# Optimization experiments

Measured on AMD Instinct MI355X. Metric: run time of the kernel, lower is better.

Reference implementation:

```python
import jax, jax.numpy as jnp
import numpy as np

B, T, F, H, E = 256, 512, 32, 512, 32
NUM_TICKERS, PREDICT_DAYS = 5000, 30


def setup_inputs() -> dict:
    key = jax.random.key(0)
    ks = jax.random.split(key, 16)
    s = 0.05  # small init scale for stability
    return {
        "ticker_id": jax.random.randint(ks[0], (B,), 0, NUM_TICKERS),
        "sequence": jax.random.normal(ks[1], (B, T, F), jnp.float32),
        "embed_table": jax.random.normal(ks[2], (NUM_TICKERS, E), jnp.float32) * s,
        "Wih0": jax.random.normal(ks[3], (3 * H, F), jnp.float32) * s,
        "Whh0": jax.random.normal(ks[4], (3 * H, H), jnp.float32) * s,
        "bih0": jax.random.normal(ks[5], (3 * H,), jnp.float32) * s,
        "bhh0": jax.random.normal(ks[6], (3 * H,), jnp.float32) * s,
        "Wih1": jax.random.normal(ks[7], (3 * H, H), jnp.float32) * s,
        "Whh1": jax.random.normal(ks[8], (3 * H, H), jnp.float32) * s,
        "bih1": jax.random.normal(ks[9], (3 * H,), jnp.float32) * s,
        "bhh1": jax.random.normal(ks[10], (3 * H,), jnp.float32) * s,
        "fc1_w": jax.random.normal(ks[11], (H, H + E), jnp.float32) * s,
        "fc1_b": jax.random.normal(ks[12], (H,), jnp.float32) * s,
        "fc2_w": jax.random.normal(ks[13], (PREDICT_DAYS, H), jnp.float32) * s,
        "fc2_b": jax.random.normal(ks[14], (PREDICT_DAYS,), jnp.float32) * s,
    }


def _gru_layer(x, Wih, Whh, bih, bhh):
    """Standard torch-convention GRU layer. x: (B,T,in) -> (B,T,H), h_last (B,H).
    Gate packing along 3H axis: [r, z, n]."""
    Hs = Whh.shape[1]
    # precompute input projections for all timesteps in one GEMM
    gx = jnp.einsum('btf,gf->tbg', x, Wih) + bih  # (T,B,3H)

    def step(h, gxt):
        gh = h @ Whh.T + bhh                         # (B,3H)
        r = jax.nn.sigmoid(gxt[:, :Hs] + gh[:, :Hs])
        z = jax.nn.sigmoid(gxt[:, Hs:2 * Hs] + gh[:, Hs:2 * Hs])
        n = jnp.tanh(gxt[:, 2 * Hs:] + r * gh[:, 2 * Hs:])
        h_new = (1.0 - z) * n + z * h
        return h_new, h_new

    h0 = jnp.zeros((x.shape[0], Hs), x.dtype)
    h_last, ys = jax.lax.scan(step, h0, gx)          # ys: (T,B,H)
    return jnp.moveaxis(ys, 0, 1), h_last


def reference(ticker_id, sequence, embed_table, Wih0, Whh0, bih0, bhh0,
              Wih1, Whh1, bih1, bhh1, fc1_w, fc1_b, fc2_w, fc2_b):
    out0, _ = _gru_layer(sequence, Wih0, Whh0, bih0, bhh0)
    _, h_last = _gru_layer(out0, Wih1, Whh1, bih1, bhh1)   # top-layer final hidden (B,H)
    embed = embed_table[ticker_id]                          # (B,E)
    h = jnp.concatenate([h_last, embed], axis=1)            # (B,H+E)
    h = jax.nn.relu(h @ fc1_w.T + fc1_b)                    # dropout is eval no-op
    return h @ fc2_w.T + fc2_b                              # (B, predict_days)
```

## Files before the change

### kernel.cpp

```cpp
#include <hip/hip_runtime.h>
#include <hip/hip_bf16.h>


namespace {
constexpr int kB  = 256;
constexpr int kT  = 512;
constexpr int kF  = 32;
constexpr int kH  = 512;
constexpr int kE  = 32;
constexpr int kPD = 30;

constexpr int GBLK = 256;
constexpr int NTHR = 256;
constexpr int RG   = 32;
constexpr int HB   = 16;

constexpr int IMG  = kB * kH * 2;
constexpr int RING = 8;

constexpr int PART_OFF = 0;
constexpr int PARTN    = 1536;
constexpr int LDSB     = 98304;
static_assert(LDSB <= 160 * 1024, "LDS overflow");

constexpr size_t WS_CNT   = 0;
constexpr size_t WS_TOTAL = 1024;
constexpr size_t WS_FB    = 1152;
constexpr size_t WS_FLG1  = 2048;
constexpr size_t WS_FLG0  = 4096;
constexpr size_t WS_H0B   = 65536;
constexpr size_t WS_H1B   = WS_H0B + (size_t)RING * IMG;
constexpr size_t WS_H1F   = WS_H1B + (size_t)RING * IMG;
constexpr size_t WS_INIT  = WS_H1F;

typedef __bf16 bf16_t;
typedef __bf16 bf16x8 __attribute__((ext_vector_type(8)));
typedef float  f32x4  __attribute__((ext_vector_type(4)));

#define MFMA __builtin_amdgcn_mfma_f32_16x16x32_bf16
#define LDSF4(p) (*(__attribute__((address_space(3))) f32x4*)(p))

#define WAITVM(N)                                              \
  do {                                                         \
    asm volatile("s_waitcnt vmcnt(" #N ")" ::: "memory");      \
    __builtin_amdgcn_sched_barrier(0);                         \
  } while (0)

__device__ __forceinline__ float sigmoid_f(float x) {
  return 1.f / (1.f + __expf(-x));
}
__device__ __forceinline__ float tanh_f(float x) {
  float a = fabsf(x);
  float e = __expf(-2.f * a);
  float t = (1.f - e) / (1.f + e);
  return copysignf(t, x);
}

__device__ __forceinline__ bf16x8 ld16a(const char* p) {
  bf16x8 v;
  asm volatile("global_load_dwordx4 %0, %1, off"
               : "=v"(v) : "v"(p) : "memory");
  return v;
}

__device__ __forceinline__ bf16x8 fragf(const float* p) {
  bf16x8 t;
#pragma unroll
  for (int j = 0; j < 8; ++j) t[j] = (bf16_t)p[j];
  return t;
}

__device__ __forceinline__ bf16x8 ld16_mall(const bf16_t* p) {
  const unsigned long long* q = (const unsigned long long*)p;
  unsigned long long lo =
      __hip_atomic_load(q, __ATOMIC_RELAXED, __HIP_MEMORY_SCOPE_AGENT);
  unsigned long long hi =
      __hip_atomic_load(q + 1, __ATOMIC_RELAXED, __HIP_MEMORY_SCOPE_AGENT);
  union { unsigned long long u[2]; bf16x8 v; } x;
  x.u[0] = lo; x.u[1] = hi;
  return x.v;
}

__device__ __forceinline__ void st2_mall(bf16_t* p, float v) {
  bf16_t b = (bf16_t)v;
  unsigned short bits = __builtin_bit_cast(unsigned short, b);
  __hip_atomic_store((unsigned short*)p, bits, __ATOMIC_RELAXED,
                     __HIP_MEMORY_SCOPE_AGENT);
}
template <bool XL>
__device__ __forceinline__ void st2x(bf16_t* p, float v) {
  if constexpr (XL) *p = (bf16_t)v;
  else st2_mall(p, v);
}

__device__ __forceinline__ void drain_stores() {
  asm volatile("s_waitcnt vmcnt(0)" ::: "memory");
}

__device__ __forceinline__ unsigned ld_flag_sc1(const unsigned* p) {
  unsigned v;
  asm volatile("global_load_dword %0, %1, off sc1\n\ts_waitcnt vmcnt(0)"
               : "=v"(v) : "v"(p) : "memory");
  return v;
}

template <bool XL>
__device__ __forceinline__ void poll_flags(const unsigned* base, int idx,
                                           unsigned tgt) {
  const unsigned* fp = base + idx;
  long guard = 0;
  if constexpr (XL) {
    for (;;) {
      unsigned v = ld_flag_sc1(fp);
      if (__all((int)(v >= tgt))) break;
      if (++guard > (1L << 22)) break;
    }
  } else {
    for (;;) {
      unsigned v = __hip_atomic_load(fp, __ATOMIC_RELAXED,
                                     __HIP_MEMORY_SCOPE_AGENT);
      if (__all((int)(v >= tgt))) break;
      __builtin_amdgcn_s_sleep(1);
      if (++guard > (1L << 20)) break;
    }
  }
}

template <bool XL>
__device__ __forceinline__ void flag_post(unsigned* p, unsigned tgt) {
  if constexpr (XL) {
    *(volatile unsigned*)p = tgt;
  } else {
    __hip_atomic_store(p, tgt, __ATOMIC_RELAXED, __HIP_MEMORY_SCOPE_AGENT);
  }
}
}


#define L0_ISSUE(buf, base)                                         \
  _Pragma("unroll") for (int j = 0; j < 4; ++j)                     \
      buf[j] = ld16a(hsrc + (base + j) * 1024)
#define L0_MFMA(buf, base)                                          \
  _Pragma("unroll") for (int j = 0; j < 4; ++j) {                   \
    aR  = MFMA(buf[j], f0[0][base + j], aR, 0, 0, 0);               \
    aZ  = MFMA(buf[j], f0[1][base + j], aZ, 0, 0, 0);               \
    aNH = MFMA(buf[j], f0[2][base + j], aNH, 0, 0, 0);              \
  }
#define L1_ISSUE(b0, b1, base)                                      \
  _Pragma("unroll") for (int j = 0; j < 4; ++j) {                   \
    b0[j] = ld16a(hsrc + (base + j) * 1024);                        \
    b1[j] = ld16a(hsrc + 16384 + (base + j) * 1024);                \
  }
#define L1_MFMA(acc0, acc1, acc2, w, b0, b1, base)                  \
  _Pragma("unroll") for (int j = 0; j < 4; ++j) {                   \
    acc0[0] = MFMA(b0[j], w[0][base + j], acc0[0], 0, 0, 0);        \
    acc0[1] = MFMA(b1[j], w[0][base + j], acc0[1], 0, 0, 0);        \
    acc1[0] = MFMA(b0[j], w[1][base + j], acc1[0], 0, 0, 0);        \
    acc1[1] = MFMA(b1[j], w[1][base + j], acc1[1], 0, 0, 0);        \
    acc2[0] = MFMA(b0[j], w[2][base + j], acc2[0], 0, 0, 0);        \
    acc2[1] = MFMA(b1[j], w[2][base + j], acc2[1], 0, 0, 0);        \
  }

template <bool XL>
__device__ __attribute__((noinline)) void role_l0(
    const float* __restrict__ seq, const float* __restrict__ Whh0,
    const float* __restrict__ Wih0, bf16_t* __restrict__ h0b,
    unsigned* __restrict__ flg0p, int g, int slot, int lane, int rbase,
    int rt, int c, float b0r, float b0z, float b0nx, float b0nh) {
  const int lm = lane & 15, lq = lane >> 4, koff = lq * 8;
  const int arow = rbase + rt * 16 + lm;

  bf16x8 f0[3][17];
#pragma unroll
  for (int gg = 0; gg < 3; ++gg) {
    const float* wh = Whh0 + (size_t)(gg * kH + c) * kH + koff;
#pragma unroll
    for (int kc = 0; kc < 16; ++kc) f0[gg][kc] = fragf(wh + kc * 32);
    f0[gg][16] = fragf(Wih0 + (size_t)(gg * kH + c) * kF + koff);
  }
  float h0m[4] = {0.f, 0.f, 0.f, 0.f};

  const int kcb = slot >> 1;
  const int lq2 = ((slot & 1) << 1) | (lm >> 3);
  const int stoff = ((g * 2 + rt) * 16 + kcb) * 1024 +
                    ((lq2 << 4) + lq * 4) * 16 + (lm & 7) * 2;
  const int tbase = (g * 2 + rt) * 16 * 1024;

  for (int s = 0; s <= kT; ++s) {
    const int pr = (s + RING - 1) & (RING - 1), pw = s & (RING - 1);
    if (s < kT) {
      const float* xp = seq + ((size_t)arow * kT + s) * kF + koff;
      float xs[8];
#pragma unroll
      for (int j = 0; j < 8; ++j) xs[j] = xp[j];
      if (s > 0) poll_flags<XL>(flg0p, lane, (unsigned)s);
      if constexpr (XL) {
        if ((s & (RING - 1)) == 0) asm volatile("buffer_inv" ::: "memory");
      }
      f32x4 aR{0,0,0,0}, aZ{0,0,0,0}, aNH{0,0,0,0}, aNX{0,0,0,0};
      const char* hsrc = (const char*)h0b + pr * IMG + tbase + lane * 16;
      if constexpr (XL) {
        bf16x8 cA[4], cB[4];
        L0_ISSUE(cA, 0);
        L0_ISSUE(cB, 4);
        WAITVM(4);
        L0_MFMA(cA, 0);
        L0_ISSUE(cA, 8);
        WAITVM(4);
        L0_MFMA(cB, 4);
        L0_ISSUE(cB, 12);
        WAITVM(4);
        L0_MFMA(cA, 8);
        WAITVM(0);
        L0_MFMA(cB, 12);
      } else {
#pragma unroll
        for (int kc = 0; kc < 16; ++kc) {
          bf16x8 a = ld16_mall((const bf16_t*)(hsrc + kc * 1024));
          aR  = MFMA(a, f0[0][kc], aR, 0, 0, 0);
          aZ  = MFMA(a, f0[1][kc], aZ, 0, 0, 0);
          aNH = MFMA(a, f0[2][kc], aNH, 0, 0, 0);
        }
      }
      {
        bf16x8 ax;
#pragma unroll
        for (int j = 0; j < 8; ++j) ax[j] = (bf16_t)xs[j];
        aR  = MFMA(ax, f0[0][16], aR, 0, 0, 0);
        aZ  = MFMA(ax, f0[1][16], aZ, 0, 0, 0);
        aNX = MFMA(ax, f0[2][16], aNX, 0, 0, 0);
      }
      char* hnb = (char*)h0b + pw * IMG;
#pragma unroll
      for (int i = 0; i < 4; ++i) {
        float r = sigmoid_f(aR[i] + b0r);
        float z = sigmoid_f(aZ[i] + b0z);
        float n = tanh_f((aNX[i] + b0nx) + r * (aNH[i] + b0nh));
        float hn = (1.f - z) * n + z * h0m[i];
        h0m[i] = hn;
        st2x<XL>((bf16_t*)(hnb + stoff + i * 16), hn);
      }
      drain_stores();
      if (lane == 0) flag_post<XL>(flg0p + rt * 32 + slot, (unsigned)(s + 1));
    }
    __syncthreads();
    if constexpr (!XL) __syncthreads();
  }
}

template <bool XL>
__device__ __attribute__((noinline)) void role_l1h(
    const float* __restrict__ Whh1, bf16_t* __restrict__ h1b,
    float* __restrict__ h1f, unsigned* __restrict__ flg1p, int slot,
    float* part, int g, int lane, int rbase, int c,
    float b1r, float b1z, float b1nx, float b1nh) {
  const int lm = lane & 15, lq = lane >> 4, koff = lq * 8;
  bf16x8 fh[3][16];
#pragma unroll
  for (int gg = 0; gg < 3; ++gg) {
    const float* wh = Whh1 + (size_t)(gg * kH + c) * kH + koff;
#pragma unroll
    for (int kc = 0; kc < 16; ++kc) fh[gg][kc] = fragf(wh + kc * 32);
  }
  float h1m[2][4] = {{0,0,0,0},{0,0,0,0}};

  const int kcb = slot >> 1;
  const int lq2 = ((slot & 1) << 1) | (lm >> 3);
  const int st0 = (g * 2 * 16 + kcb) * 1024 +
                  ((lq2 << 4) + lq * 4) * 16 + (lm & 7) * 2;
  const int tbase = g * 2 * 16 * 1024;

  for (int s = 0; s <= kT; ++s) {
    const int pr = (s + RING - 1) & (RING - 1), pw = s & (RING - 1);
    f32x4 cR[2], cZ[2], cNH[2];
#pragma unroll
    for (int rt = 0; rt < 2; ++rt) {
      cR[rt] = f32x4{0,0,0,0}; cZ[rt] = f32x4{0,0,0,0}; cNH[rt] = f32x4{0,0,0,0};
    }
    if (s >= 1) {
      poll_flags<XL>(flg1p, lane & 31, (unsigned)s);
      if constexpr (XL) {
        if ((s & (RING - 1)) == 0) asm volatile("buffer_inv" ::: "memory");
      }
      const char* hsrc = (const char*)h1b + pr * IMG + tbase + lane * 16;
      if constexpr (XL) {
        bf16x8 a0A[4], a1A[4], a0B[4], a1B[4];
        L1_ISSUE(a0A, a1A, 0);
        L1_ISSUE(a0B, a1B, 4);
        WAITVM(8);
        L1_MFMA(cR, cZ, cNH, fh, a0A, a1A, 0);
        L1_ISSUE(a0A, a1A, 8);
        WAITVM(8);
        L1_MFMA(cR, cZ, cNH, fh, a0B, a1B, 4);
        L1_ISSUE(a0B, a1B, 12);
        WAITVM(8);
        L1_MFMA(cR, cZ, cNH, fh, a0A, a1A, 8);
        WAITVM(0);
        L1_MFMA(cR, cZ, cNH, fh, a0B, a1B, 12);
      } else {
#pragma unroll
        for (int kc = 0; kc < 16; ++kc) {
          bf16x8 a0 = ld16_mall((const bf16_t*)(hsrc + kc * 1024));
          bf16x8 a1 = ld16_mall((const bf16_t*)(hsrc + 16384 + kc * 1024));
          cR[0]  = MFMA(a0, fh[0][kc], cR[0], 0,0,0);
          cR[1]  = MFMA(a1, fh[0][kc], cR[1], 0,0,0);
          cZ[0]  = MFMA(a0, fh[1][kc], cZ[0], 0,0,0);
          cZ[1]  = MFMA(a1, fh[1][kc], cZ[1], 0,0,0);
          cNH[0] = MFMA(a0, fh[2][kc], cNH[0],0,0,0);
          cNH[1] = MFMA(a1, fh[2][kc], cNH[1],0,0,0);
        }
      }
    }
    __syncthreads();
    if (s >= 1) {
      float* pb = part + (s & 1) * PARTN;
      char* hnb = (char*)h1b + pw * IMG;
#pragma unroll
      for (int rt = 0; rt < 2; ++rt) {
        f32x4 pR  = LDSF4(pb + ((rt * 3 + 0) * 64 + lane) * 4);
        f32x4 pZ  = LDSF4(pb + ((rt * 3 + 1) * 64 + lane) * 4);
        f32x4 pNX = LDSF4(pb + ((rt * 3 + 2) * 64 + lane) * 4);
#pragma unroll
        for (int i = 0; i < 4; ++i) {
          float r = sigmoid_f(cR[rt][i] + pR[i] + b1r);
          float z = sigmoid_f(cZ[rt][i] + pZ[i] + b1z);
          float n = tanh_f((pNX[i] + b1nx) + r * (cNH[rt][i] + b1nh));
          float hn = (1.f - z) * n + z * h1m[rt][i];
          h1m[rt][i] = hn;
          if (s < kT) st2x<XL>((bf16_t*)(hnb + st0 + rt * 16384 + i * 16), hn);
          else        h1f[(rbase + rt * 16 + lq * 4 + i) * kH + c] = hn;
        }
      }
    }
    if (s < kT) {
      drain_stores();
      if (lane == 0) flag_post<XL>(flg1p + slot, (unsigned)(s + 1));
    }
    if constexpr (!XL) {
      if (s < kT) poll_flags<XL>(flg1p, lane & 31, (unsigned)(s + 1));
      __syncthreads();
    }
  }
}

template <bool XL>
__device__ __attribute__((noinline)) void role_l1x(
    const float* __restrict__ Wih1, bf16_t* __restrict__ h0b,
    float* part, unsigned* __restrict__ flg0p, int g, int lane, int c) {
  const int lq = lane >> 4, koff = lq * 8;
  bf16x8 fx[3][16];
#pragma unroll
  for (int gg = 0; gg < 3; ++gg) {
    const float* wi = Wih1 + (size_t)(gg * kH + c) * kH + koff;
#pragma unroll
    for (int kc = 0; kc < 16; ++kc) fx[gg][kc] = fragf(wi + kc * 32);
  }
  const int tbase = g * 2 * 16 * 1024;

  for (int s = 0; s <= kT; ++s) {
    const int pr = (s + RING - 1) & (RING - 1);
    if (s >= 1) {
      poll_flags<XL>(flg0p, lane, (unsigned)s);
      if constexpr (XL) {
        if ((s & (RING - 1)) == 0) asm volatile("buffer_inv" ::: "memory");
      }
      f32x4 xR[2], xZ[2], xNX[2];
#pragma unroll
      for (int rt = 0; rt < 2; ++rt) {
        xR[rt] = f32x4{0,0,0,0}; xZ[rt] = f32x4{0,0,0,0}; xNX[rt] = f32x4{0,0,0,0};
      }
      const char* hsrc = (const char*)h0b + pr * IMG + tbase + lane * 16;
      if constexpr (XL) {
        bf16x8 a0A[4], a1A[4], a0B[4], a1B[4];
        L1_ISSUE(a0A, a1A, 0);
        L1_ISSUE(a0B, a1B, 4);
        WAITVM(8);
        L1_MFMA(xR, xZ, xNX, fx, a0A, a1A, 0);
        L1_ISSUE(a0A, a1A, 8);
        WAITVM(8);
        L1_MFMA(xR, xZ, xNX, fx, a0B, a1B, 4);
        L1_ISSUE(a0B, a1B, 12);
        WAITVM(8);
        L1_MFMA(xR, xZ, xNX, fx, a0A, a1A, 8);
        WAITVM(0);
        L1_MFMA(xR, xZ, xNX, fx, a0B, a1B, 12);
      } else {
#pragma unroll
        for (int kc = 0; kc < 16; ++kc) {
          bf16x8 a0 = ld16_mall((const bf16_t*)(hsrc + kc * 1024));
          bf16x8 a1 = ld16_mall((const bf16_t*)(hsrc + 16384 + kc * 1024));
          xR[0]  = MFMA(a0, fx[0][kc], xR[0], 0,0,0);
          xR[1]  = MFMA(a1, fx[0][kc], xR[1], 0,0,0);
          xZ[0]  = MFMA(a0, fx[1][kc], xZ[0], 0,0,0);
          xZ[1]  = MFMA(a1, fx[1][kc], xZ[1], 0,0,0);
          xNX[0] = MFMA(a0, fx[2][kc], xNX[0],0,0,0);
          xNX[1] = MFMA(a1, fx[2][kc], xNX[1],0,0,0);
        }
      }
      float* pb = part + (s & 1) * PARTN;
#pragma unroll
      for (int rt = 0; rt < 2; ++rt) {
        LDSF4(pb + ((rt * 3 + 0) * 64 + lane) * 4) = xR[rt];
        LDSF4(pb + ((rt * 3 + 1) * 64 + lane) * 4) = xZ[rt];
        LDSF4(pb + ((rt * 3 + 2) * 64 + lane) * 4) = xNX[rt];
      }
    }
    __syncthreads();
    if constexpr (!XL) __syncthreads();
  }
}

__launch_bounds__(NTHR, 1)
__global__ void gru_persistent(
    const float* __restrict__ seq,
    const float* __restrict__ Wih0, const float* __restrict__ Whh0,
    const float* __restrict__ bih0, const float* __restrict__ bhh0,
    const float* __restrict__ Wih1, const float* __restrict__ Whh1,
    const float* __restrict__ bih1, const float* __restrict__ bhh1,
    char* __restrict__ ws) {
  extern __shared__ char smem[];
  float* part = (float*)(smem + PART_OFF);
  __shared__ unsigned sh_enc;

  const int tid = threadIdx.x;

  if (tid == 0) {
    unsigned xcd;
    asm("s_getreg_b32 %0, hwreg(HW_REG_XCC_ID)" : "=s"(xcd));
    xcd &= 7;
    unsigned* cnt   = (unsigned*)(ws + WS_CNT) + xcd * 32;
    unsigned* total = (unsigned*)(ws + WS_TOTAL);
    unsigned* fb    = (unsigned*)(ws + WS_FB);
    unsigned slot = __hip_atomic_fetch_add(cnt, 1u, __ATOMIC_RELAXED,
                                           __HIP_MEMORY_SCOPE_AGENT);
    if (slot >= 32)
      __hip_atomic_store(fb, 1u, __ATOMIC_RELAXED, __HIP_MEMORY_SCOPE_AGENT);
    __hip_atomic_fetch_add(total, 1u, __ATOMIC_RELAXED,
                           __HIP_MEMORY_SCOPE_AGENT);
    long guard = 0;
    while (__hip_atomic_load(total, __ATOMIC_RELAXED,
                             __HIP_MEMORY_SCOPE_AGENT) < (unsigned)GBLK) {
      __builtin_amdgcn_s_sleep(1);
      if (++guard > (1L << 24)) break;
    }
    unsigned f = __hip_atomic_load(fb, __ATOMIC_RELAXED,
                                   __HIP_MEMORY_SCOPE_AGENT);
    sh_enc = (f << 31) | (xcd << 8) | (slot & 255);
  }
  __syncthreads();
  const unsigned enc = sh_enc;
  const bool fallback = (enc >> 31) != 0;
  const int g    = fallback ? (blockIdx.x & 7)  : (int)((enc >> 8) & 7);
  const int slot = fallback ? (blockIdx.x >> 3) : (int)(enc & 255);
  const int hs   = slot * HB;

  const int lm = tid & 15;
  const int c = hs + lm;
  const float b0r  = bih0[c] + bhh0[c];
  const float b0z  = bih0[kH + c] + bhh0[kH + c];
  const float b0nx = bih0[2 * kH + c];
  const float b0nh = bhh0[2 * kH + c];
  const float b1r  = bih1[c] + bhh1[c];
  const float b1z  = bih1[kH + c] + bhh1[kH + c];
  const float b1nx = bih1[2 * kH + c];
  const float b1nh = bhh1[2 * kH + c];

  bf16_t* h0b = (bf16_t*)(ws + WS_H0B);
  bf16_t* h1b = (bf16_t*)(ws + WS_H1B);
  float*  h1f = (float*)(ws + WS_H1F);
  unsigned* flg1p = (unsigned*)(ws + WS_FLG1) + g * 32;
  unsigned* flg0p = (unsigned*)(ws + WS_FLG0) + g * 64;
  const int wv   = tid >> 6;
  const int lane = tid & 63;
  const int rbase = g * RG;

  if (!fallback) {
    if (wv == 0)
      role_l0<true>(seq, Whh0, Wih0, h0b, flg0p, g, slot, lane, rbase, 0, c,
                    b0r, b0z, b0nx, b0nh);
    else if (wv == 2)
      role_l0<true>(seq, Whh0, Wih0, h0b, flg0p, g, slot, lane, rbase, 1, c,
                    b0r, b0z, b0nx, b0nh);
    else if (wv == 1)
      role_l1h<true>(Whh1, h1b, h1f, flg1p, slot, part, g, lane, rbase, c,
                     b1r, b1z, b1nx, b1nh);
    else
      role_l1x<true>(Wih1, h0b, part, flg0p, g, lane, c);
  } else {
    if (wv == 0)
      role_l0<false>(seq, Whh0, Wih0, h0b, flg0p, g, slot, lane, rbase, 0, c,
                     b0r, b0z, b0nx, b0nh);
    else if (wv == 2)
      role_l0<false>(seq, Whh0, Wih0, h0b, flg0p, g, slot, lane, rbase, 1, c,
                     b0r, b0z, b0nx, b0nh);
    else if (wv == 1)
      role_l1h<false>(Whh1, h1b, h1f, flg1p, slot, part, g, lane, rbase, c,
                      b1r, b1z, b1nx, b1nh);
    else
      role_l1x<false>(Wih1, h0b, part, flg0p, g, lane, c);
  }
}

__global__ void head_kernel(const float* __restrict__ h1,
                            const int* __restrict__ ticker,
                            const float* __restrict__ etab,
                            const float* __restrict__ fc1w,
                            const float* __restrict__ fc1b,
                            const float* __restrict__ fc2w,
                            const float* __restrict__ fc2b,
                            float* __restrict__ out) {
  __shared__ float xin[4][kH + kE];
  __shared__ float y1[4][kH];
  const int tid = threadIdx.x;
  const int b0 = blockIdx.x * 4;

  for (int idx = tid; idx < 4 * (kH + kE); idx += 256) {
    const int r = idx / (kH + kE), k = idx % (kH + kE);
    const int b = b0 + r;
    xin[r][k] = (k < kH) ? h1[b * kH + k] : etab[ticker[b] * kE + (k - kH)];
  }
  __syncthreads();

#pragma unroll
  for (int jj = 0; jj < 2; ++jj) {
    const int j = tid + jj * 256;
    const float* wr = fc1w + j * (kH + kE);
    float a0 = 0.f, a1 = 0.f, a2 = 0.f, a3 = 0.f;
    for (int k = 0; k < kH + kE; ++k) {
      const float w = wr[k];
      a0 += w * xin[0][k];
      a1 += w * xin[1][k];
      a2 += w * xin[2][k];
      a3 += w * xin[3][k];
    }
    const float bb = fc1b[j];
    y1[0][j] = fmaxf(a0 + bb, 0.f);
    y1[1][j] = fmaxf(a1 + bb, 0.f);
    y1[2][j] = fmaxf(a2 + bb, 0.f);
    y1[3][j] = fmaxf(a3 + bb, 0.f);
  }
  __syncthreads();

  if (tid < 4 * kPD) {
    const int r = tid / kPD, j = tid % kPD;
    const float* wr = fc2w + j * kH;
    float acc = fc2b[j];
    for (int k = 0; k < kH; ++k) acc += wr[k] * y1[r][k];
    out[(b0 + r) * kPD + j] = acc;
  }
}

extern "C" void kernel_launch(void* const* d_in, const int* in_sizes, int n_in,
                              void* d_out, int out_size, void* d_ws,
                              size_t ws_size, hipStream_t stream) {
  (void)in_sizes; (void)n_in; (void)out_size; (void)ws_size;

  const int*   ticker = (const int*)d_in[0];
  const float* seq    = (const float*)d_in[1];
  const float* etab   = (const float*)d_in[2];
  const float* Wih0   = (const float*)d_in[3];
  const float* Whh0   = (const float*)d_in[4];
  const float* bih0   = (const float*)d_in[5];
  const float* bhh0   = (const float*)d_in[6];
  const float* Wih1   = (const float*)d_in[7];
  const float* Whh1   = (const float*)d_in[8];
  const float* bih1   = (const float*)d_in[9];
  const float* bhh1   = (const float*)d_in[10];
  const float* fc1w   = (const float*)d_in[11];
  const float* fc1b   = (const float*)d_in[12];
  const float* fc2w   = (const float*)d_in[13];
  const float* fc2b   = (const float*)d_in[14];

  char* ws = (char*)d_ws;
  (void)hipMemsetAsync(ws, 0, WS_INIT, stream);

  gru_persistent<<<GBLK, NTHR, LDSB, stream>>>(
      seq, Wih0, Whh0, bih0, bhh0, Wih1, Whh1, bih1, bhh1, ws);

  head_kernel<<<kB / 4, 256, 0, stream>>>((const float*)(ws + WS_H1F), ticker,
                                          etab, fc1w, fc1b, fc2w, fc2b,
                                          (float*)d_out);
}
```

Before: 2.178 ms.

## Replace per-step block barriers with LDS flag handoff and ring-reuse global flags

Drops the per-timestep __syncthreads that coupled the layer-0, layer-1 hidden and layer-1 input waves in the fast path. The layer-1 partial-sum exchange now uses LDS ready/consumed counters, and layer 0 waits on a new global flag array before overwriting ring slots, so waves can run ahead up to the ring depth. It also issues buffer_inv every step instead of every eighth. The intent is to remove barrier stalls between roles on the recurrent critical path, at the cost of extra flag polling, more cache invalidations and added risk of memory-ordering bugs.

```diff
diff --git a/kernel.cpp b/kernel.cpp
--- a/kernel.cpp
+++ b/kernel.cpp
@@ -20,6 +20,7 @@
 
 constexpr int PART_OFF = 0;
 constexpr int PARTN    = 1536;
+constexpr int PF_OFF   = 16384;
 constexpr int LDSB     = 98304;
 static_assert(LDSB <= 160 * 1024, "LDS overflow");
 
@@ -28,6 +29,7 @@
 constexpr size_t WS_FB    = 1152;
 constexpr size_t WS_FLG1  = 2048;
 constexpr size_t WS_FLG0  = 4096;
+constexpr size_t WS_FLG3  = 6144;
 constexpr size_t WS_H0B   = 65536;
 constexpr size_t WS_H1B   = WS_H0B + (size_t)RING * IMG;
 constexpr size_t WS_H1F   = WS_H1B + (size_t)RING * IMG;
@@ -39,6 +41,7 @@
 
 #define MFMA __builtin_amdgcn_mfma_f32_16x16x32_bf16
 #define LDSF4(p) (*(__attribute__((address_space(3))) f32x4*)(p))
+#define LDSVU(p) (*(volatile __attribute__((address_space(3))) unsigned*)(p))
 
 #define WAITVM(N)                                              \
   do {                                                         \
@@ -126,6 +129,27 @@
   }
 }
 
+__device__ __forceinline__ void poll_l0(const unsigned* f0,
+                                        const unsigned* f3, int lane,
+                                        unsigned s) {
+  unsigned t3 = (s > 6u) ? s - 6u : 0u;
+  const unsigned* p0 = f0 + lane;
+  const unsigned* p3 = f3 + (lane & 31);
+  const bool chk3 = lane < 32;
+  long guard = 0;
+  for (;;) {
+    unsigned v0, v3;
+    asm volatile(
+        "global_load_dword %0, %2, off sc1\n\t"
+        "global_load_dword %1, %3, off sc1\n\t"
+        "s_waitcnt vmcnt(0)"
+        : "=v"(v0), "=v"(v3) : "v"(p0), "v"(p3) : "memory");
+    bool ok = (v0 >= s) && (!chk3 || v3 >= t3);
+    if (__all((int)ok)) break;
+    if (++guard > (1L << 22)) break;
+  }
+}
+
 template <bool XL>
 __device__ __forceinline__ void flag_post(unsigned* p, unsigned tgt) {
   if constexpr (XL) {
@@ -133,6 +157,14 @@
   } else {
     __hip_atomic_store(p, tgt, __ATOMIC_RELAXED, __HIP_MEMORY_SCOPE_AGENT);
   }
+}
+
+__device__ __forceinline__ void lds_poll(unsigned* p, unsigned tgt) {
+  long guard = 0;
+  while (LDSVU(p) < tgt) {
+    if (++guard > (1L << 22)) break;
+  }
+  asm volatile("" ::: "memory");
 }
 }
 
@@ -165,8 +197,9 @@
 __device__ __attribute__((noinline)) void role_l0(
     const float* __restrict__ seq, const float* __restrict__ Whh0,
     const float* __restrict__ Wih0, bf16_t* __restrict__ h0b,
-    unsigned* __restrict__ flg0p, int g, int slot, int lane, int rbase,
-    int rt, int c, float b0r, float b0z, float b0nx, float b0nh) {
+    unsigned* __restrict__ flg0p, unsigned* __restrict__ flg3p,
+    int g, int slot, int lane, int rbase, int rt, int c,
+    float b0r, float b0z, float b0nx, float b0nh) {
   const int lm = lane & 15, lq = lane >> 4, koff = lq * 8;
   const int arow = rbase + rt * 16 + lm;
 
@@ -186,74 +219,77 @@
                     ((lq2 << 4) + lq * 4) * 16 + (lm & 7) * 2;
   const int tbase = (g * 2 + rt) * 16 * 1024;
 
-  for (int s = 0; s <= kT; ++s) {
+  for (int s = 0; s < kT; ++s) {
     const int pr = (s + RING - 1) & (RING - 1), pw = s & (RING - 1);
-    if (s < kT) {
-      const float* xp = seq + ((size_t)arow * kT + s) * kF + koff;
-      float xs[8];
-#pragma unroll
-      for (int j = 0; j < 8; ++j) xs[j] = xp[j];
+    const float* xp = seq + ((size_t)arow * kT + s) * kF + koff;
+    float xs[8];
+#pragma unroll
+    for (int j = 0; j < 8; ++j) xs[j] = xp[j];
+    if constexpr (XL) {
+      if (s > 0) poll_l0(flg0p, flg3p, lane, (unsigned)s);
+      asm volatile("buffer_inv" ::: "memory");
+    } else {
       if (s > 0) poll_flags<XL>(flg0p, lane, (unsigned)s);
-      if constexpr (XL) {
-        if ((s & (RING - 1)) == 0) asm volatile("buffer_inv" ::: "memory");
-      }
-      f32x4 aR{0,0,0,0}, aZ{0,0,0,0}, aNH{0,0,0,0}, aNX{0,0,0,0};
-      const char* hsrc = (const char*)h0b + pr * IMG + tbase + lane * 16;
-      if constexpr (XL) {
-        bf16x8 cA[4], cB[4];
-        L0_ISSUE(cA, 0);
-        L0_ISSUE(cB, 4);
-        WAITVM(4);
-        L0_MFMA(cA, 0);
-        L0_ISSUE(cA, 8);
-        WAITVM(4);
-        L0_MFMA(cB, 4);
-        L0_ISSUE(cB, 12);
-        WAITVM(4);
-        L0_MFMA(cA, 8);
-        WAITVM(0);
-        L0_MFMA(cB, 12);
-      } else {
-#pragma unroll
-        for (int kc = 0; kc < 16; ++kc) {
-          bf16x8 a = ld16_mall((const bf16_t*)(hsrc + kc * 1024));
-          aR  = MFMA(a, f0[0][kc], aR, 0, 0, 0);
-          aZ  = MFMA(a, f0[1][kc], aZ, 0, 0, 0);
-          aNH = MFMA(a, f0[2][kc], aNH, 0, 0, 0);
-        }
-      }
-      {
-        bf16x8 ax;
-#pragma unroll
-        for (int j = 0; j < 8; ++j) ax[j] = (bf16_t)xs[j];
-        aR  = MFMA(ax, f0[0][16], aR, 0, 0, 0);
-        aZ  = MFMA(ax, f0[1][16], aZ, 0, 0, 0);
-        aNX = MFMA(ax, f0[2][16], aNX, 0, 0, 0);
-      }
-      char* hnb = (char*)h0b + pw * IMG;
-#pragma unroll
-      for (int i = 0; i < 4; ++i) {
-        float r = sigmoid_f(aR[i] + b0r);
-        float z = sigmoid_f(aZ[i] + b0z);
-        float n = tanh_f((aNX[i] + b0nx) + r * (aNH[i] + b0nh));
-        float hn = (1.f - z) * n + z * h0m[i];
-        h0m[i] = hn;
-        st2x<XL>((bf16_t*)(hnb + stoff + i * 16), hn);
-      }
-      drain_stores();
-      if (lane == 0) flag_post<XL>(flg0p + rt * 32 + slot, (unsigned)(s + 1));
-    }
-    __syncthreads();
-    if constexpr (!XL) __syncthreads();
-  }
+    }
+    f32x4 aR{0,0,0,0}, aZ{0,0,0,0}, aNH{0,0,0,0}, aNX{0,0,0,0};
+    const char* hsrc = (const char*)h0b + pr * IMG + tbase + lane * 16;
+    if constexpr (XL) {
+      bf16x8 cA[4], cB[4];
+      L0_ISSUE(cA, 0);
+      L0_ISSUE(cB, 4);
+      WAITVM(4);
+      L0_MFMA(cA, 0);
+      L0_ISSUE(cA, 8);
+      WAITVM(4);
+      L0_MFMA(cB, 4);
+      L0_ISSUE(cB, 12);
+      WAITVM(4);
+      L0_MFMA(cA, 8);
+      WAITVM(0);
+      L0_MFMA(cB, 12);
+    } else {
+#pragma unroll
+      for (int kc = 0; kc < 16; ++kc) {
+        bf16x8 a = ld16_mall((const bf16_t*)(hsrc + kc * 1024));
+        aR  = MFMA(a, f0[0][kc], aR, 0, 0, 0);
+        aZ  = MFMA(a, f0[1][kc], aZ, 0, 0, 0);
+        aNH = MFMA(a, f0[2][kc], aNH, 0, 0, 0);
+      }
+    }
+    {
+      bf16x8 ax;
+#pragma unroll
+      for (int j = 0; j < 8; ++j) ax[j] = (bf16_t)xs[j];
+      aR  = MFMA(ax, f0[0][16], aR, 0, 0, 0);
+      aZ  = MFMA(ax, f0[1][16], aZ, 0, 0, 0);
+      aNX = MFMA(ax, f0[2][16], aNX, 0, 0, 0);
+    }
+    char* hnb = (char*)h0b + pw * IMG;
+#pragma unroll
+    for (int i = 0; i < 4; ++i) {
+      float r = sigmoid_f(aR[i] + b0r);
+      float z = sigmoid_f(aZ[i] + b0z);
+      float n = tanh_f((aNX[i] + b0nx) + r * (aNH[i] + b0nh));
+      float hn = (1.f - z) * n + z * h0m[i];
+      h0m[i] = hn;
+      st2x<XL>((bf16_t*)(hnb + stoff + i * 16), hn);
+    }
+    drain_stores();
+    if (lane == 0) flag_post<XL>(flg0p + rt * 32 + slot, (unsigned)(s + 1));
+    if constexpr (!XL) {
+      __syncthreads();
+      __syncthreads();
+    }
+  }
+  if constexpr (!XL) { __syncthreads(); __syncthreads(); }
 }
 
 template <bool XL>
 __device__ __attribute__((noinline)) void role_l1h(
     const float* __restrict__ Whh1, bf16_t* __restrict__ h1b,
     float* __restrict__ h1f, unsigned* __restrict__ flg1p, int slot,
-    float* part, int g, int lane, int rbase, int c,
-    float b1r, float b1z, float b1nx, float b1nh) {
+    float* part, unsigned* pf_ready, unsigned* pf_cons, int g, int lane,
+    int rbase, int c, float b1r, float b1z, float b1nx, float b1nh) {
   const int lm = lane & 15, lq = lane >> 4, koff = lq * 8;
   bf16x8 fh[3][16];
 #pragma unroll
@@ -272,15 +308,15 @@
 
   for (int s = 0; s <= kT; ++s) {
     const int pr = (s + RING - 1) & (RING - 1), pw = s & (RING - 1);
-    f32x4 cR[2], cZ[2], cNH[2];
-#pragma unroll
-    for (int rt = 0; rt < 2; ++rt) {
-      cR[rt] = f32x4{0,0,0,0}; cZ[rt] = f32x4{0,0,0,0}; cNH[rt] = f32x4{0,0,0,0};
-    }
     if (s >= 1) {
+      f32x4 cR[2], cZ[2], cNH[2];
+#pragma unroll
+      for (int rt = 0; rt < 2; ++rt) {
+        cR[rt] = f32x4{0,0,0,0}; cZ[rt] = f32x4{0,0,0,0}; cNH[rt] = f32x4{0,0,0,0};
+      }
       poll_flags<XL>(flg1p, lane & 31, (unsigned)s);
       if constexpr (XL) {
-        if ((s & (RING - 1)) == 0) asm volatile("buffer_inv" ::: "memory");
+        asm volatile("buffer_inv" ::: "memory");
       }
       const char* hsrc = (const char*)h1b + pr * IMG + tbase + lane * 16;
       if constexpr (XL) {
@@ -310,9 +346,11 @@
           cNH[1] = MFMA(a1, fh[2][kc], cNH[1],0,0,0);
         }
       }
-    }
-    __syncthreads();
-    if (s >= 1) {
+      if constexpr (XL) {
+        lds_poll(pf_ready, (unsigned)s);
+      } else {
+        __syncthreads();
+      }
       float* pb = part + (s & 1) * PARTN;
       char* hnb = (char*)h1b + pw * IMG;
 #pragma unroll
@@ -331,6 +369,9 @@
           else        h1f[(rbase + rt * 16 + lq * 4 + i) * kH + c] = hn;
         }
       }
+      if (s < kT && lane == 0) LDSVU(pf_cons) = (unsigned)s;
+    } else {
+      if constexpr (!XL) __syncthreads();
     }
     if (s < kT) {
       drain_stores();
@@ -346,7 +387,8 @@
 template <bool XL>
 __device__ __attribute__((noinline)) void role_l1x(
     const float* __restrict__ Wih1, bf16_t* __restrict__ h0b,
-    float* part, unsigned* __restrict__ flg0p, int g, int lane, int c) {
+    float* part, unsigned* __restrict__ flg0p, unsigned* __restrict__ flg3p,
+    unsigned* pf_ready, unsigned* pf_cons, int g, int slot, int lane, int c) {
   const int lq = lane >> 4, koff = lq * 8;
   bf16x8 fx[3][16];
 #pragma unroll
@@ -362,7 +404,7 @@
     if (s >= 1) {
       poll_flags<XL>(flg0p, lane, (unsigned)s);
       if constexpr (XL) {
-        if ((s & (RING - 1)) == 0) asm volatile("buffer_inv" ::: "memory");
+        asm volatile("buffer_inv" ::: "memory");
       }
       f32x4 xR[2], xZ[2], xNX[2];
 #pragma unroll
@@ -383,6 +425,7 @@
         WAITVM(8);
         L1_MFMA(xR, xZ, xNX, fx, a0A, a1A, 8);
         WAITVM(0);
+        if (lane == 0) flag_post<XL>(flg3p + slot, (unsigned)(s + 1));
         L1_MFMA(xR, xZ, xNX, fx, a0B, a1B, 12);
       } else {
 #pragma unroll
@@ -397,6 +440,9 @@
           xNX[1] = MFMA(a1, fx[2][kc], xNX[1],0,0,0);
         }
       }
+      if constexpr (XL) {
+        if (s >= 2) lds_poll(pf_cons, (unsigned)(s - 1));
+      }
       float* pb = part + (s & 1) * PARTN;
 #pragma unroll
       for (int rt = 0; rt < 2; ++rt) {
@@ -404,9 +450,15 @@
         LDSF4(pb + ((rt * 3 + 1) * 64 + lane) * 4) = xZ[rt];
         LDSF4(pb + ((rt * 3 + 2) * 64 + lane) * 4) = xNX[rt];
       }
-    }
-    __syncthreads();
-    if constexpr (!XL) __syncthreads();
+      if constexpr (XL) {
+        asm volatile("s_waitcnt lgkmcnt(0)" ::: "memory");
+        if (lane == 0) LDSVU(pf_ready) = (unsigned)s;
+      }
+    }
+    if constexpr (!XL) {
+      __syncthreads();
+      __syncthreads();
+    }
   }
 }
 
@@ -420,11 +472,15 @@
     char* __restrict__ ws) {
   extern __shared__ char smem[];
   float* part = (float*)(smem + PART_OFF);
+  unsigned* pf_ready = (unsigned*)(smem + PF_OFF);
+  unsigned* pf_cons  = (unsigned*)(smem + PF_OFF + 128);
   __shared__ unsigned sh_enc;
 
   const int tid = threadIdx.x;
 
   if (tid == 0) {
+    LDSVU(pf_ready) = 0u;
+    LDSVU(pf_cons)  = 0u;
     unsigned xcd;
     asm("s_getreg_b32 %0, hwreg(HW_REG_XCC_ID)" : "=s"(xcd));
     xcd &= 7;
@@ -470,34 +526,37 @@
   float*  h1f = (float*)(ws + WS_H1F);
   unsigned* flg1p = (unsigned*)(ws + WS_FLG1) + g * 32;
   unsigned* flg0p = (unsigned*)(ws + WS_FLG0) + g * 64;
+  unsigned* flg3p = (unsigned*)(ws + WS_FLG3) + g * 32;
   const int wv   = tid >> 6;
   const int lane = tid & 63;
   const int rbase = g * RG;
 
   if (!fallback) {
     if (wv == 0)
-      role_l0<true>(seq, Whh0, Wih0, h0b, flg0p, g, slot, lane, rbase, 0, c,
-                    b0r, b0z, b0nx, b0nh);
+      role_l0<true>(seq, Whh0, Wih0, h0b, flg0p, flg3p, g, slot, lane, rbase,
+                    0, c, b0r, b0z, b0nx, b0nh);
     else if (wv == 2)
-      role_l0<true>(seq, Whh0, Wih0, h0b, flg0p, g, slot, lane, rbase, 1, c,
-                    b0r, b0z, b0nx, b0nh);
+      role_l0<true>(seq, Whh0, Wih0, h0b, flg0p, flg3p, g, slot, lane, rbase,
+                    1, c, b0r, b0z, b0nx, b0nh);
     else if (wv == 1)
-      role_l1h<true>(Whh1, h1b, h1f, flg1p, slot, part, g, lane, rbase, c,
-                     b1r, b1z, b1nx, b1nh);
+      role_l1h<true>(Whh1, h1b, h1f, flg1p, slot, part, pf_ready, pf_cons, g,
+                     lane, rbase, c, b1r, b1z, b1nx, b1nh);
     else
-      role_l1x<true>(Wih1, h0b, part, flg0p, g, lane, c);
+      role_l1x<true>(Wih1, h0b, part, flg0p, flg3p, pf_ready, pf_cons, g,
+                     slot, lane, c);
   } else {
     if (wv == 0)
-      role_l0<false>(seq, Whh0, Wih0, h0b, flg0p, g, slot, lane, rbase, 0, c,
-                     b0r, b0z, b0nx, b0nh);
+      role_l0<false>(seq, Whh0, Wih0, h0b, flg0p, flg3p, g, slot, lane, rbase,
+                     0, c, b0r, b0z, b0nx, b0nh);
     else if (wv == 2)
-      role_l0<false>(seq, Whh0, Wih0, h0b, flg0p, g, slot, lane, rbase, 1, c,
-                     b0r, b0z, b0nx, b0nh);
+      role_l0<false>(seq, Whh0, Wih0, h0b, flg0p, flg3p, g, slot, lane, rbase,
+                     1, c, b0r, b0z, b0nx, b0nh);
     else if (wv == 1)
-      role_l1h<false>(Whh1, h1b, h1f, flg1p, slot, part, g, lane, rbase, c,
-                      b1r, b1z, b1nx, b1nh);
+      role_l1h<false>(Whh1, h1b, h1f, flg1p, slot, part, pf_ready, pf_cons, g,
+                      lane, rbase, c, b1r, b1z, b1nx, b1nh);
     else
-      role_l1x<false>(Wih1, h0b, part, flg0p, g, lane, c);
+      role_l1x<false>(Wih1, h0b, part, flg0p, flg3p, pf_ready, pf_cons, g,
+                      slot, lane, c);
   }
 }
 
```

Result: slower. 4.045 ms (+85.7%).
